# Performance work log

Measured on AMD Instinct MI355X. Metric: run time of the kernel, lower is better.

## Reference

```python
import jax, jax.numpy as jnp
import numpy as np

D = 1024
H = 16
DH = D // H
F = 4096
EPS = 1e-5

def layernorm(x, gamma, beta):
    mean = jnp.mean(x, axis=-1, keepdims=True)
    var = jnp.mean((x - mean) ** 2, axis=-1, keepdims=True)  # biased variance
    return gamma * (x - mean) / jnp.sqrt(var + EPS) + beta

def setup_inputs() -> dict:
    key = jax.random.key(0)
    ks = jax.random.split(key, 12)
    s = 1.0 / np.sqrt(D)
    sf = 1.0 / np.sqrt(F)
    return {
        "x": jax.random.normal(ks[0], (16, 512, D), dtype=jnp.float32),
        "Wq": jax.random.normal(ks[1], (H, D, DH), dtype=jnp.float32) * s,
        "Wk": jax.random.normal(ks[2], (H, D, DH), dtype=jnp.float32) * s,
        "Wv": jax.random.normal(ks[3], (H, D, DH), dtype=jnp.float32) * s,
        "Wo": jax.random.normal(ks[4], (D, D), dtype=jnp.float32) * s,
        "bo": jax.random.normal(ks[5], (D,), dtype=jnp.float32) * s,
        "gamma1": jnp.ones((D,), dtype=jnp.float32),
        "beta1": jnp.zeros((D,), dtype=jnp.float32),
        "gamma2": jnp.ones((D,), dtype=jnp.float32),
        "beta2": jnp.zeros((D,), dtype=jnp.float32),
        "W1": jax.random.normal(ks[6], (D, F), dtype=jnp.float32) * s,
        "b1": jax.random.normal(ks[7], (F,), dtype=jnp.float32) * s,
        "W2": jax.random.normal(ks[8], (F, D), dtype=jnp.float32) * sf,
        "b2": jax.random.normal(ks[9], (D,), dtype=jnp.float32) * sf,
    }

def reference(x, Wq, Wk, Wv, Wo, bo, gamma1, beta1, gamma2, beta2, W1, b1, W2, b2):
    B, S, _ = x.shape
    n1 = layernorm(x, gamma1, beta1)
    # per-head projections (no bias) -> [B,H,S,DH]
    Q = jnp.einsum('bsd,hde->bhse', n1, Wq)
    K = jnp.einsum('bsd,hde->bhse', n1, Wk)
    V = jnp.einsum('bsd,hde->bhse', n1, Wv)
    scores = jnp.einsum('bhse,bhte->bhst', Q, K) / jnp.sqrt(jnp.float32(DH))
    causal = jnp.tril(jnp.ones((S, S), dtype=bool))  # keep lower triangle
    scores = jnp.where(causal, scores, -jnp.inf)
    attn = jax.nn.softmax(scores, axis=-1)  # dropout is identity at eval
    heads = jnp.einsum('bhst,bhte->bhse', attn, V)
    concat = heads.transpose(0, 2, 1, 3).reshape(B, S, D)  # concat heads in order
    x = x + (concat @ Wo + bo)
    n2 = layernorm(x, gamma2, beta2)
    ff = jax.nn.gelu(n2 @ W1 + b1, approximate=False) @ W2 + b2
    return x + ff
```

## Files before the change

### kernel.cpp

```cpp
#include <hip/hip_runtime.h>
#include <hip/hip_bf16.h>
#include <math.h>

constexpr int Dm = 1024;
constexpr int Hh = 16;
constexpr int Ff = 4096;
constexpr int Ss = 512;
constexpr int Bbatch = 16;
constexpr int NT = Bbatch * Ss;
constexpr float EPSc = 1e-5f;

typedef __attribute__((ext_vector_type(8))) short bfrag;
typedef __attribute__((ext_vector_type(4))) float f32x4;

static __device__ __forceinline__ float gelu_f(float v) {
    const float u = v * (0.7978845608f + 0.0356774081f * v * v);
    const float e = __expf(2.0f * u);
    const float th = 1.0f - 2.0f / (e + 1.0f);
    return 0.5f * v * (1.0f + th);
}

static __device__ __forceinline__ void gload16(const void* g, void* l) {
    __builtin_amdgcn_global_load_lds((__attribute__((address_space(1))) void*)g,
                                     (__attribute__((address_space(3))) void*)l,
                                     16, 0, 0);
}

#define SWZ(row, colb) ((row) * 128 + ((colb) ^ (((row) & 7) << 4)))

__global__ void __launch_bounds__(256) transpose_cvt(const float* __restrict__ in,
                                                     __hip_bfloat16* __restrict__ out,
                                                     int R, int C,
                                                     long in_zs, long out_zs) {
    __shared__ float tile[32][33];
    const float* inz = in + (size_t)blockIdx.z * in_zs;
    __hip_bfloat16* outz = out + (size_t)blockIdx.z * out_zs;
    const int c0 = blockIdx.x * 32, r0 = blockIdx.y * 32;
    const int tx = threadIdx.x & 31, ty4 = (threadIdx.x >> 5) * 4;
    #pragma unroll
    for (int i = 0; i < 4; i++)
        tile[ty4 + i][tx] = inz[(size_t)(r0 + ty4 + i) * C + c0 + tx];
    __syncthreads();
    #pragma unroll
    for (int i = 0; i < 4; i++)
        outz[(size_t)(c0 + ty4 + i) * R + r0 + tx] = __float2bfloat16(tile[tx][ty4 + i]);
}

__global__ void __launch_bounds__(256) ln_bf16(const float* __restrict__ x,
                                               const float* __restrict__ gamma,
                                               const float* __restrict__ beta,
                                               __hip_bfloat16* __restrict__ out) {
    const int row = blockIdx.x;
    const int tid = threadIdx.x;
    const int lane = tid & 63, w = tid >> 6;
    float4 xv = reinterpret_cast<const float4*>(x + (size_t)row * Dm)[tid];
    float s  = xv.x + xv.y + xv.z + xv.w;
    float ss = xv.x * xv.x + xv.y * xv.y + xv.z * xv.z + xv.w * xv.w;
    #pragma unroll
    for (int o = 32; o > 0; o >>= 1) {
        s  += __shfl_down(s,  o, 64);
        ss += __shfl_down(ss, o, 64);
    }
    __shared__ float red[2][4];
    if (lane == 0) { red[0][w] = s; red[1][w] = ss; }
    __syncthreads();
    float st  = red[0][0] + red[0][1] + red[0][2] + red[0][3];
    float sst = red[1][0] + red[1][1] + red[1][2] + red[1][3];
    float mean = st * (1.0f / Dm);
    float var  = sst * (1.0f / Dm) - mean * mean;
    float inv  = rsqrtf(var + EPSc);
    float4 g = reinterpret_cast<const float4*>(gamma)[tid];
    float4 b = reinterpret_cast<const float4*>(beta)[tid];
    __hip_bfloat16 t[4] __attribute__((aligned(8)));
    t[0] = __float2bfloat16((xv.x - mean) * inv * g.x + b.x);
    t[1] = __float2bfloat16((xv.y - mean) * inv * g.y + b.y);
    t[2] = __float2bfloat16((xv.z - mean) * inv * g.z + b.z);
    t[3] = __float2bfloat16((xv.w - mean) * inv * g.w + b.w);
    *reinterpret_cast<ushort4*>(out + (size_t)row * Dm + tid * 4) =
        *reinterpret_cast<ushort4*>(t);
}

template<int EPI>
__global__ void __launch_bounds__(256) gemm_db(const __hip_bfloat16* __restrict__ A, int lda,
                                               const __hip_bfloat16* __restrict__ Bt, int ldb,
                                               const float* __restrict__ bias,
                                               const float* __restrict__ res,
                                               void* __restrict__ Cout, int ldc,
                                               int nbx, int K) {
    __shared__ __hip_bfloat16 As[2][128 * 64];
    __shared__ __hip_bfloat16 Bs[2][128 * 64];
    const int tid = threadIdx.x, l = tid & 63, w = tid >> 6;
    const int lr = l & 15, lg = l >> 4;
    const int nwg = gridDim.x;
    const int sbid = (blockIdx.x & 7) * (nwg >> 3) + (blockIdx.x >> 3);
    const int bx = sbid % nbx, by = sbid / nbx;
    const int m0 = by * 128, n0 = bx * 128;
    const int wr = w >> 1, wc = w & 1;
    const int srow = l >> 3;
    const int scol = ((l & 7) ^ srow) * 8;
    const int NK = K >> 6;

    auto STAGE = [&](int t, int bsel) {
        const int k0 = t * 64;
        #pragma unroll
        for (int j = 0; j < 4; j++) {
            const int rb = w * 32 + j * 8;
            gload16(A  + (size_t)(m0 + rb + srow) * lda + k0 + scol, &As[bsel][rb * 64]);
            gload16(Bt + (size_t)(n0 + rb + srow) * ldb + k0 + scol, &Bs[bsel][rb * 64]);
        }
    };

    f32x4 acc[4][4] = {};
    STAGE(0, 0);
    for (int t = 0; t < NK; t++) {
        const int cur = t & 1;
        if (t + 1 < NK) {
            STAGE(t + 1, cur ^ 1);
            asm volatile("s_waitcnt vmcnt(8)" ::: "memory");
        } else {
            asm volatile("s_waitcnt vmcnt(0)" ::: "memory");
        }
        __builtin_amdgcn_s_barrier();
        __builtin_amdgcn_sched_barrier(0);
        const char* Ab = (const char*)&As[cur][0];
        const char* Bb = (const char*)&Bs[cur][0];
        #pragma unroll
        for (int kk = 0; kk < 2; kk++) {
            bfrag a[4], b[4];
            #pragma unroll
            for (int mi = 0; mi < 4; mi++) {
                const int row = wr * 64 + mi * 16 + lr;
                a[mi] = *(const bfrag*)(Ab + SWZ(row, (kk * 4 + lg) * 16));
            }
            #pragma unroll
            for (int ni = 0; ni < 4; ni++) {
                const int row = wc * 64 + ni * 16 + lr;
                b[ni] = *(const bfrag*)(Bb + SWZ(row, (kk * 4 + lg) * 16));
            }
            __builtin_amdgcn_s_setprio(1);
            #pragma unroll
            for (int mi = 0; mi < 4; mi++)
                #pragma unroll
                for (int ni = 0; ni < 4; ni++)
                    acc[mi][ni] = __builtin_amdgcn_mfma_f32_16x16x32_bf16(a[mi], b[ni], acc[mi][ni], 0, 0, 0);
            __builtin_amdgcn_s_setprio(0);
        }
        __builtin_amdgcn_sched_barrier(0);
        __builtin_amdgcn_s_barrier();
    }
    const int rb = m0 + wr * 64 + lg * 4;
    const int cb = n0 + wc * 64 + lr;
    #pragma unroll
    for (int mi = 0; mi < 4; mi++) {
        #pragma unroll
        for (int ni = 0; ni < 4; ni++) {
            #pragma unroll
            for (int rg = 0; rg < 4; rg++) {
                const int row = rb + mi * 16 + rg;
                const int col = cb + ni * 16;
                const size_t off = (size_t)row * ldc + col;
                const float v = acc[mi][ni][rg];
                if (EPI == 0) {
                    ((__hip_bfloat16*)Cout)[off] = __float2bfloat16(v);
                } else if (EPI == 1) {
                    ((float*)Cout)[off] = v + bias[col] + res[off];
                } else if (EPI == 2) {
                    ((__hip_bfloat16*)Cout)[off] = __float2bfloat16(gelu_f(v + bias[col]));
                } else {
                    ((float*)Cout)[off] = ((float*)Cout)[off] + v + bias[col];
                }
            }
        }
    }
}

__global__ void __launch_bounds__(256) attn_mfma(const __hip_bfloat16* __restrict__ QKV,
                                                 __hip_bfloat16* __restrict__ Oc) {
    constexpr int LDQ = 3072;
    __shared__ __hip_bfloat16 Qs[64 * 64];
    __shared__ __hip_bfloat16 Ks[64 * 64];
    __shared__ __hip_bfloat16 Vts[64 * 64];
    __shared__ __hip_bfloat16 Ps[4][16 * 64];
    const int tid = threadIdx.x, l = tid & 63, w = tid >> 6;
    const int lr = l & 15, lg = l >> 4;
    const int qt = blockIdx.x & 7;
    const int h  = (blockIdx.x >> 3) & 15;
    const int b  = blockIdx.x >> 7;

    const __hip_bfloat16* Qg = QKV + (size_t)(b * Ss + qt * 64) * LDQ + h * 64;
    const __hip_bfloat16* Kg = QKV + (size_t)(b * Ss) * LDQ + 1024 + h * 64;
    const __hip_bfloat16* Vg = QKV + (size_t)(b * Ss) * LDQ + 2048 + h * 64;

    const int r8 = l >> 3;
    const int scol = 8 * ((l & 7) ^ r8);

    #pragma unroll
    for (int j = 0; j < 2; j++) {
        const int slot = w * 2 + j;
        gload16(Qg + (size_t)(slot * 8 + r8) * LDQ + scol, Qs + slot * 512);
    }

    float m_run[4] = {-1e30f, -1e30f, -1e30f, -1e30f};
    float l_run[4] = {0.f, 0.f, 0.f, 0.f};
    f32x4 acc_o[4] = {};

    for (int kt = 0; kt <= qt; ++kt) {
        __syncthreads();
        #pragma unroll
        for (int j = 0; j < 2; j++) {
            const int slot = w * 2 + j;
            gload16(Kg + (size_t)(kt * 64 + slot * 8 + r8) * LDQ + scol, Ks + slot * 512);
        }
        unsigned short* vt = reinterpret_cast<unsigned short*>(Vts);
        #pragma unroll
        for (int j = 0; j < 2; j++) {
            const int e = tid + j * 256;
            const int key = e >> 3, f0 = (e & 7) * 8;
            const uint4 raw = *reinterpret_cast<const uint4*>(
                Vg + (size_t)(kt * 64 + key) * LDQ + f0);
            const unsigned int rw[4] = {raw.x, raw.y, raw.z, raw.w};
            #pragma unroll
            for (int e2 = 0; e2 < 8; e2++) {
                const int feat = f0 + e2;
                const int ad = feat * 128 + ((key * 2) ^ ((feat & 7) << 4));
                vt[ad >> 1] = (unsigned short)(rw[e2 >> 1] >> ((e2 & 1) * 16));
            }
        }
        __syncthreads();

        f32x4 s4[4] = {};
        #pragma unroll
        for (int kk = 0; kk < 2; kk++) {
            const bfrag aq = *reinterpret_cast<const bfrag*>(
                (const char*)Qs + SWZ(w * 16 + lr, kk * 64 + lg * 16));
            #pragma unroll
            for (int ni = 0; ni < 4; ni++) {
                const bfrag bk = *reinterpret_cast<const bfrag*>(
                    (const char*)Ks + SWZ(ni * 16 + lr, kk * 64 + lg * 16));
                s4[ni] = __builtin_amdgcn_mfma_f32_16x16x32_bf16(aq, bk, s4[ni], 0, 0, 0);
            }
        }
        float p[4][4];
        #pragma unroll
        for (int ni = 0; ni < 4; ni++)
            #pragma unroll
            for (int rg = 0; rg < 4; rg++)
                p[ni][rg] = s4[ni][rg] * 0.125f;
        if (kt == qt) {
            #pragma unroll
            for (int ni = 0; ni < 4; ni++)
                #pragma unroll
                for (int rg = 0; rg < 4; rg++)
                    if (ni * 16 + lr > w * 16 + lg * 4 + rg) p[ni][rg] = -1e30f;
        }
        float sf[4];
        #pragma unroll
        for (int rg = 0; rg < 4; rg++) {
            float mx = fmaxf(fmaxf(p[0][rg], p[1][rg]), fmaxf(p[2][rg], p[3][rg]));
            #pragma unroll
            for (int o = 1; o < 16; o <<= 1) mx = fmaxf(mx, __shfl_xor(mx, o, 64));
            const float mn = fmaxf(m_run[rg], mx);
            sf[rg] = __expf(m_run[rg] - mn);
            m_run[rg] = mn;
        }
        float rsum[4] = {};
        #pragma unroll
        for (int ni = 0; ni < 4; ni++)
            #pragma unroll
            for (int rg = 0; rg < 4; rg++) {
                const float e = __expf(p[ni][rg] - m_run[rg]);
                p[ni][rg] = e;
                rsum[rg] += e;
            }
        #pragma unroll
        for (int rg = 0; rg < 4; rg++) {
            #pragma unroll
            for (int o = 1; o < 16; o <<= 1) rsum[rg] += __shfl_xor(rsum[rg], o, 64);
            l_run[rg] = l_run[rg] * sf[rg] + rsum[rg];
        }
        #pragma unroll
        for (int di = 0; di < 4; di++)
            #pragma unroll
            for (int rg = 0; rg < 4; rg++)
                acc_o[di][rg] *= sf[rg];
        unsigned short* pw = reinterpret_cast<unsigned short*>(Ps[w]);
        #pragma unroll
        for (int ni = 0; ni < 4; ni++)
            #pragma unroll
            for (int rg = 0; rg < 4; rg++) {
                const int prow = lg * 4 + rg;
                const int ad = SWZ(prow, (ni * 16 + lr) * 2);
                __hip_bfloat16 pb = __float2bfloat16(p[ni][rg]);
                pw[ad >> 1] = *reinterpret_cast<unsigned short*>(&pb);
            }
        #pragma unroll
        for (int kk = 0; kk < 2; kk++) {
            const bfrag pa = *reinterpret_cast<const bfrag*>(
                (const char*)Ps[w] + SWZ(lr, kk * 64 + lg * 16));
            #pragma unroll
            for (int di = 0; di < 4; di++) {
                const bfrag vb = *reinterpret_cast<const bfrag*>(
                    (const char*)Vts + SWZ(di * 16 + lr, kk * 64 + lg * 16));
                acc_o[di] = __builtin_amdgcn_mfma_f32_16x16x32_bf16(pa, vb, acc_o[di], 0, 0, 0);
            }
        }
    }
    #pragma unroll
    for (int di = 0; di < 4; di++)
        #pragma unroll
        for (int rg = 0; rg < 4; rg++) {
            const int q = qt * 64 + w * 16 + lg * 4 + rg;
            const float v = acc_o[di][rg] / l_run[rg];
            Oc[(size_t)(b * Ss + q) * Dm + h * 64 + di * 16 + lr] = __float2bfloat16(v);
        }
}

extern "C" void kernel_launch(void* const* d_in, const int* in_sizes, int n_in,
                              void* d_out, int out_size, void* d_ws, size_t ws_size,
                              hipStream_t stream) {
    const float* x   = (const float*)d_in[0];
    const float* Wq  = (const float*)d_in[1];
    const float* Wk  = (const float*)d_in[2];
    const float* Wv  = (const float*)d_in[3];
    const float* Wo  = (const float*)d_in[4];
    const float* bo  = (const float*)d_in[5];
    const float* g1  = (const float*)d_in[6];
    const float* be1 = (const float*)d_in[7];
    const float* g2  = (const float*)d_in[8];
    const float* be2 = (const float*)d_in[9];
    const float* W1  = (const float*)d_in[10];
    const float* b1  = (const float*)d_in[11];
    const float* W2  = (const float*)d_in[12];
    const float* b2  = (const float*)d_in[13];
    float* out = (float*)d_out;

    char* wsb = (char*)d_ws;
    __hip_bfloat16* WqkvT = (__hip_bfloat16*)(wsb);
    __hip_bfloat16* WoT   = (__hip_bfloat16*)(wsb + 6291456);
    __hip_bfloat16* W1T   = (__hip_bfloat16*)(wsb + 8388608);
    __hip_bfloat16* W2T   = (__hip_bfloat16*)(wsb + 16777216);
    __hip_bfloat16* n1    = (__hip_bfloat16*)(wsb + 25165824);
    __hip_bfloat16* QKV   = (__hip_bfloat16*)(wsb + 41943040);
    __hip_bfloat16* concat = n1;
    __hip_bfloat16* n2     = n1;
    __hip_bfloat16* h1     = QKV;

    transpose_cvt<<<dim3(2, 32, 16), 256, 0, stream>>>(Wq, WqkvT,              1024, 64, 65536, 65536);
    transpose_cvt<<<dim3(2, 32, 16), 256, 0, stream>>>(Wk, WqkvT + 1024 * 1024, 1024, 64, 65536, 65536);
    transpose_cvt<<<dim3(2, 32, 16), 256, 0, stream>>>(Wv, WqkvT + 2048 * 1024, 1024, 64, 65536, 65536);
    transpose_cvt<<<dim3(32, 32, 1), 256, 0, stream>>>(Wo, WoT, 1024, 1024, 0, 0);
    transpose_cvt<<<dim3(128, 32, 1), 256, 0, stream>>>(W1, W1T, 1024, 4096, 0, 0);
    transpose_cvt<<<dim3(32, 128, 1), 256, 0, stream>>>(W2, W2T, 4096, 1024, 0, 0);

    ln_bf16<<<NT, 256, 0, stream>>>(x, g1, be1, n1);
    gemm_db<0><<<1536, 256, 0, stream>>>(n1, Dm, WqkvT, Dm, nullptr, nullptr,
                                         QKV, 3072, 24, Dm);
    attn_mfma<<<NT * Hh / 64, 256, 0, stream>>>(QKV, concat);
    gemm_db<1><<<512, 256, 0, stream>>>(concat, Dm, WoT, Dm, bo, x,
                                        out, Dm, 8, Dm);
    ln_bf16<<<NT, 256, 0, stream>>>(out, g2, be2, n2);
    gemm_db<2><<<2048, 256, 0, stream>>>(n2, Dm, W1T, Dm, b1, nullptr,
                                         h1, Ff, 32, Dm);
    gemm_db<3><<<512, 256, 0, stream>>>(h1, Ff, W2T, Ff, b2, nullptr,
                                        out, Dm, 8, Ff);
}
```

Measured before the change: 402.6 us.

## Prefetch GEMM tiles through registers and write V transposed from QKV epilogue

The GEMM kernel no longer uses double-buffered direct global-to-LDS loads. It now prefetches the next K-tile into registers while the current single-buffered LDS tile is consumed, which halves LDS use and may allow more resident blocks. The QKV projection gains a new epilogue that writes Q/K as before and writes V already transposed per head, so the attention kernel can load V with async 16-byte LDS loads instead of an element-wise transpose scatter. In exchange, the register prefetch adds VGPR pressure, and the V epilogue does narrow 8-byte strided stores.

```diff
diff --git a/kernel.cpp b/kernel.cpp
--- a/kernel.cpp
+++ b/kernel.cpp
@@ -81,14 +81,15 @@
 }
 
 template<int EPI>
-__global__ void __launch_bounds__(256) gemm_db(const __hip_bfloat16* __restrict__ A, int lda,
+__global__ void __launch_bounds__(256) gemm_rp(const __hip_bfloat16* __restrict__ A, int lda,
                                                const __hip_bfloat16* __restrict__ Bt, int ldb,
                                                const float* __restrict__ bias,
                                                const float* __restrict__ res,
                                                void* __restrict__ Cout, int ldc,
+                                               __hip_bfloat16* __restrict__ Vt,
                                                int nbx, int K) {
-    __shared__ __hip_bfloat16 As[2][128 * 64];
-    __shared__ __hip_bfloat16 Bs[2][128 * 64];
+    __shared__ __hip_bfloat16 As[128 * 64];
+    __shared__ __hip_bfloat16 Bs[128 * 64];
     const int tid = threadIdx.x, l = tid & 63, w = tid >> 6;
     const int lr = l & 15, lg = l >> 4;
     const int nwg = gridDim.x;
@@ -100,42 +101,49 @@
     const int scol = ((l & 7) ^ srow) * 8;
     const int NK = K >> 6;
 
-    auto STAGE = [&](int t, int bsel) {
+    uint4 pa[4], pb[4];
+    auto LOADREG = [&](int t) {
         const int k0 = t * 64;
         #pragma unroll
         for (int j = 0; j < 4; j++) {
             const int rb = w * 32 + j * 8;
-            gload16(A  + (size_t)(m0 + rb + srow) * lda + k0 + scol, &As[bsel][rb * 64]);
-            gload16(Bt + (size_t)(n0 + rb + srow) * ldb + k0 + scol, &Bs[bsel][rb * 64]);
+            pa[j] = *(const uint4*)(A  + (size_t)(m0 + rb + srow) * lda + k0 + scol);
+            pb[j] = *(const uint4*)(Bt + (size_t)(n0 + rb + srow) * ldb + k0 + scol);
         }
     };
+    auto WRITELDS = [&]() {
+        #pragma unroll
+        for (int j = 0; j < 4; j++) {
+            const int rb = w * 32 + j * 8;
+            *(uint4*)((char*)As + rb * 128 + l * 16) = pa[j];
+            *(uint4*)((char*)Bs + rb * 128 + l * 16) = pb[j];
+        }
+    };
 
     f32x4 acc[4][4] = {};
-    STAGE(0, 0);
+    LOADREG(0);
+    asm volatile("s_waitcnt vmcnt(0)" ::: "memory");
+    __builtin_amdgcn_sched_barrier(0);
+    WRITELDS();
+    if (NK > 1) LOADREG(1);
+    asm volatile("s_waitcnt lgkmcnt(0)" ::: "memory");
+    __builtin_amdgcn_sched_barrier(0);
+    __builtin_amdgcn_s_barrier();
+
     for (int t = 0; t < NK; t++) {
-        const int cur = t & 1;
-        if (t + 1 < NK) {
-            STAGE(t + 1, cur ^ 1);
-            asm volatile("s_waitcnt vmcnt(8)" ::: "memory");
-        } else {
-            asm volatile("s_waitcnt vmcnt(0)" ::: "memory");
-        }
-        __builtin_amdgcn_s_barrier();
         __builtin_amdgcn_sched_barrier(0);
-        const char* Ab = (const char*)&As[cur][0];
-        const char* Bb = (const char*)&Bs[cur][0];
         #pragma unroll
         for (int kk = 0; kk < 2; kk++) {
             bfrag a[4], b[4];
             #pragma unroll
             for (int mi = 0; mi < 4; mi++) {
                 const int row = wr * 64 + mi * 16 + lr;
-                a[mi] = *(const bfrag*)(Ab + SWZ(row, (kk * 4 + lg) * 16));
+                a[mi] = *(const bfrag*)((const char*)As + SWZ(row, (kk * 4 + lg) * 16));
             }
             #pragma unroll
             for (int ni = 0; ni < 4; ni++) {
                 const int row = wc * 64 + ni * 16 + lr;
-                b[ni] = *(const bfrag*)(Bb + SWZ(row, (kk * 4 + lg) * 16));
+                b[ni] = *(const bfrag*)((const char*)Bs + SWZ(row, (kk * 4 + lg) * 16));
             }
             __builtin_amdgcn_s_setprio(1);
             #pragma unroll
@@ -147,36 +155,67 @@
         }
         __builtin_amdgcn_sched_barrier(0);
         __builtin_amdgcn_s_barrier();
-    }
+        if (t + 1 < NK) {
+            asm volatile("s_waitcnt vmcnt(0)" ::: "memory");
+            __builtin_amdgcn_sched_barrier(0);
+            WRITELDS();
+            if (t + 2 < NK) LOADREG(t + 2);
+            asm volatile("s_waitcnt lgkmcnt(0)" ::: "memory");
+            __builtin_amdgcn_sched_barrier(0);
+        }
+        __builtin_amdgcn_s_barrier();
+    }
+
     const int rb = m0 + wr * 64 + lg * 4;
     const int cb = n0 + wc * 64 + lr;
     #pragma unroll
     for (int mi = 0; mi < 4; mi++) {
         #pragma unroll
         for (int ni = 0; ni < 4; ni++) {
-            #pragma unroll
-            for (int rg = 0; rg < 4; rg++) {
-                const int row = rb + mi * 16 + rg;
-                const int col = cb + ni * 16;
-                const size_t off = (size_t)row * ldc + col;
-                const float v = acc[mi][ni][rg];
-                if (EPI == 0) {
-                    ((__hip_bfloat16*)Cout)[off] = __float2bfloat16(v);
-                } else if (EPI == 1) {
-                    ((float*)Cout)[off] = v + bias[col] + res[off];
-                } else if (EPI == 2) {
-                    ((__hip_bfloat16*)Cout)[off] = __float2bfloat16(gelu_f(v + bias[col]));
+            const int col = cb + ni * 16;
+            if (EPI == 4) {
+                const int row0 = rb + mi * 16;
+                if (col < 2048) {
+                    #pragma unroll
+                    for (int rg = 0; rg < 4; rg++)
+                        ((__hip_bfloat16*)Cout)[(size_t)(row0 + rg) * 2048 + col] =
+                            __float2bfloat16(acc[mi][ni][rg]);
                 } else {
-                    ((float*)Cout)[off] = ((float*)Cout)[off] + v + bias[col];
+                    const int dp = col - 2048, hh = dp >> 6, dd = dp & 63;
+                    const int bb = row0 >> 9, tk = row0 & 511;
+                    ushort4 t4;
+                    __hip_bfloat16 hv;
+                    hv = __float2bfloat16(acc[mi][ni][0]); t4.x = *(unsigned short*)&hv;
+                    hv = __float2bfloat16(acc[mi][ni][1]); t4.y = *(unsigned short*)&hv;
+                    hv = __float2bfloat16(acc[mi][ni][2]); t4.z = *(unsigned short*)&hv;
+                    hv = __float2bfloat16(acc[mi][ni][3]); t4.w = *(unsigned short*)&hv;
+                    *(ushort4*)(Vt + ((size_t)(bb * 16 + hh) * 64 + dd) * 512 + tk) = t4;
                 }
-            }
-        }
-    }
-}
-
-__global__ void __launch_bounds__(256) attn_mfma(const __hip_bfloat16* __restrict__ QKV,
+            } else {
+                #pragma unroll
+                for (int rg = 0; rg < 4; rg++) {
+                    const int row = rb + mi * 16 + rg;
+                    const size_t off = (size_t)row * ldc + col;
+                    const float v = acc[mi][ni][rg];
+                    if (EPI == 0) {
+                        ((__hip_bfloat16*)Cout)[off] = __float2bfloat16(v);
+                    } else if (EPI == 1) {
+                        ((float*)Cout)[off] = v + bias[col] + res[off];
+                    } else if (EPI == 2) {
+                        ((__hip_bfloat16*)Cout)[off] = __float2bfloat16(gelu_f(v + bias[col]));
+                    } else {
+                        ((float*)Cout)[off] = ((float*)Cout)[off] + v + bias[col];
+                    }
+                }
+            }
+        }
+    }
+}
+
+__global__ void __launch_bounds__(256) attn_mfma(const __hip_bfloat16* __restrict__ QK,
+                                                 const __hip_bfloat16* __restrict__ Vt,
                                                  __hip_bfloat16* __restrict__ Oc) {
-    constexpr int LDQ = 3072;
+    constexpr int LDQ = 2048;
     __shared__ __hip_bfloat16 Qs[64 * 64];
     __shared__ __hip_bfloat16 Ks[64 * 64];
     __shared__ __hip_bfloat16 Vts[64 * 64];
@@ -187,9 +226,9 @@
     const int h  = (blockIdx.x >> 3) & 15;
     const int b  = blockIdx.x >> 7;
 
-    const __hip_bfloat16* Qg = QKV + (size_t)(b * Ss + qt * 64) * LDQ + h * 64;
-    const __hip_bfloat16* Kg = QKV + (size_t)(b * Ss) * LDQ + 1024 + h * 64;
-    const __hip_bfloat16* Vg = QKV + (size_t)(b * Ss) * LDQ + 2048 + h * 64;
+    const __hip_bfloat16* Qg = QK + (size_t)(b * Ss + qt * 64) * LDQ + h * 64;
+    const __hip_bfloat16* Kg = QK + (size_t)(b * Ss) * LDQ + 1024 + h * 64;
+    const __hip_bfloat16* Vg = Vt + (size_t)(b * 16 + h) * 64 * 512;
 
     const int r8 = l >> 3;
     const int scol = 8 * ((l & 7) ^ r8);
@@ -210,21 +249,7 @@
         for (int j = 0; j < 2; j++) {
             const int slot = w * 2 + j;
             gload16(Kg + (size_t)(kt * 64 + slot * 8 + r8) * LDQ + scol, Ks + slot * 512);
-        }
-        unsigned short* vt = reinterpret_cast<unsigned short*>(Vts);
-        #pragma unroll
-        for (int j = 0; j < 2; j++) {
-            const int e = tid + j * 256;
-            const int key = e >> 3, f0 = (e & 7) * 8;
-            const uint4 raw = *reinterpret_cast<const uint4*>(
-                Vg + (size_t)(kt * 64 + key) * LDQ + f0);
-            const unsigned int rw[4] = {raw.x, raw.y, raw.z, raw.w};
-            #pragma unroll
-            for (int e2 = 0; e2 < 8; e2++) {
-                const int feat = f0 + e2;
-                const int ad = feat * 128 + ((key * 2) ^ ((feat & 7) << 4));
-                vt[ad >> 1] = (unsigned short)(rw[e2 >> 1] >> ((e2 & 1) * 16));
-            }
+            gload16(Vg + (size_t)(slot * 8 + r8) * 512 + kt * 64 + scol, Vts + slot * 512);
         }
         __syncthreads();
 
@@ -340,10 +365,11 @@
     __hip_bfloat16* W1T   = (__hip_bfloat16*)(wsb + 8388608);
     __hip_bfloat16* W2T   = (__hip_bfloat16*)(wsb + 16777216);
     __hip_bfloat16* n1    = (__hip_bfloat16*)(wsb + 25165824);
-    __hip_bfloat16* QKV   = (__hip_bfloat16*)(wsb + 41943040);
+    __hip_bfloat16* QK    = (__hip_bfloat16*)(wsb + 41943040);
+    __hip_bfloat16* Vt    = (__hip_bfloat16*)(wsb + 75497472);
     __hip_bfloat16* concat = n1;
     __hip_bfloat16* n2     = n1;
-    __hip_bfloat16* h1     = QKV;
+    __hip_bfloat16* h1     = QK;
 
     transpose_cvt<<<dim3(2, 32, 16), 256, 0, stream>>>(Wq, WqkvT,              1024, 64, 65536, 65536);
     transpose_cvt<<<dim3(2, 32, 16), 256, 0, stream>>>(Wk, WqkvT + 1024 * 1024, 1024, 64, 65536, 65536);
@@ -353,14 +379,14 @@
     transpose_cvt<<<dim3(32, 128, 1), 256, 0, stream>>>(W2, W2T, 4096, 1024, 0, 0);
 
     ln_bf16<<<NT, 256, 0, stream>>>(x, g1, be1, n1);
-    gemm_db<0><<<1536, 256, 0, stream>>>(n1, Dm, WqkvT, Dm, nullptr, nullptr,
-                                         QKV, 3072, 24, Dm);
-    attn_mfma<<<NT * Hh / 64, 256, 0, stream>>>(QKV, concat);
-    gemm_db<1><<<512, 256, 0, stream>>>(concat, Dm, WoT, Dm, bo, x,
-                                        out, Dm, 8, Dm);
+    gemm_rp<4><<<1536, 256, 0, stream>>>(n1, Dm, WqkvT, Dm, nullptr, nullptr,
+                                         QK, 2048, Vt, 24, Dm);
+    attn_mfma<<<NT * Hh / 64, 256, 0, stream>>>(QK, Vt, concat);
+    gemm_rp<1><<<512, 256, 0, stream>>>(concat, Dm, WoT, Dm, bo, x,
+                                        out, Dm, nullptr, 8, Dm);
     ln_bf16<<<NT, 256, 0, stream>>>(out, g2, be2, n2);
-    gemm_db<2><<<2048, 256, 0, stream>>>(n2, Dm, W1T, Dm, b1, nullptr,
-                                         h1, Ff, 32, Dm);
-    gemm_db<3><<<512, 256, 0, stream>>>(h1, Ff, W2T, Ff, b2, nullptr,
-                                        out, Dm, 8, Ff);
-}
+    gemm_rp<2><<<2048, 256, 0, stream>>>(n2, Dm, W1T, Dm, b1, nullptr,
+                                         h1, Ff, nullptr, 32, Dm);
+    gemm_rp<3><<<512, 256, 0, stream>>>(h1, Ff, W2T, Ff, b2, nullptr,
+                                        out, Dm, nullptr, 8, Ff);
+}
```

Result: slower. 983.3 us (+144.2%).

## Add 256x256-tile 8-wave GEMM with four-phase pipelined loads for QKV and FFN1

Applied to the files above, without the earlier changes.

Adds a new GEMM kernel that uses 512 threads and 256x256 output tiles, with double-buffered LDS. Global-to-LDS loads for the next k-steps are split across four MFMA phases, with barriers and waitcnts placed between them. The QKV projection and the FFN1+GELU GEMMs now use this kernel instead of the 128x128 one, which raises operand reuse per tile and overlaps memory traffic with compute. In exchange it uses 128KB of LDS and heavy register pressure, so only one workgroup fits per CU, and the grid has fewer blocks than there are CUs times a few.

```diff
diff --git a/kernel.cpp b/kernel.cpp
--- a/kernel.cpp
+++ b/kernel.cpp
@@ -78,6 +78,121 @@
     t[3] = __float2bfloat16((xv.w - mean) * inv * g.w + b.w);
     *reinterpret_cast<ushort4*>(out + (size_t)row * Dm + tid * 4) =
         *reinterpret_cast<ushort4*>(t);
+}
+
+template<int EPI>
+__global__ void __launch_bounds__(512, 1) gemm8ph(const __hip_bfloat16* __restrict__ A, int lda,
+                                                  const __hip_bfloat16* __restrict__ Bt, int ldb,
+                                                  const float* __restrict__ bias,
+                                                  void* __restrict__ Cout, int ldc,
+                                                  int nbx, int K) {
+    __shared__ __hip_bfloat16 As8[2][256 * 64];
+    __shared__ __hip_bfloat16 Bs8[2][256 * 64];
+    const int tid = threadIdx.x, l = tid & 63, w = tid >> 6;
+    const int lr = l & 15, lg = l >> 4;
+    const int nwg = gridDim.x;
+    const int sbid = (blockIdx.x & 7) * (nwg >> 3) + (blockIdx.x >> 3);
+    const int bx = sbid % nbx, by = sbid / nbx;
+    const int m0 = by * 256, n0 = bx * 256;
+    const int wr = w >> 2, wc = w & 3;
+    const int srow = l >> 3;
+    const int scol = ((l & 7) ^ srow) * 8;
+    const int NK = K >> 6;
+
+    auto stageA = [&](int ts, int hh) {
+        #pragma unroll
+        for (int r = 0; r < 2; r++) {
+            const int row = hh * 128 + r * 64 + w * 8 + srow;
+            gload16(A + (size_t)(m0 + row) * lda + ts * 64 + scol, &As8[ts & 1][row * 64]);
+        }
+    };
+    auto stageB = [&](int ts, int hh) {
+        #pragma unroll
+        for (int r = 0; r < 2; r++) {
+            const int row = hh * 128 + r * 64 + w * 8 + srow;
+            gload16(Bt + (size_t)(n0 + row) * ldb + ts * 64 + scol, &Bs8[ts & 1][row * 64]);
+        }
+    };
+
+    f32x4 acc[8][4] = {};
+
+    stageB(0, 0); stageB(0, 1); stageA(0, 0); stageA(0, 1);
+    stageB(1, 0); stageB(1, 1); stageA(1, 0);
+    asm volatile("s_waitcnt vmcnt(6)" ::: "memory");
+    __builtin_amdgcn_s_barrier();
+
+    for (int t = 0; t < NK; t++) {
+        const char* Ab = (const char*)&As8[t & 1][0];
+        const char* Bb = (const char*)&Bs8[t & 1][0];
+        bfrag b_[4][2];
+
+#define PH8(Q, SPRE, SPOST, VM)                                                     \
+        {                                                                           \
+            bfrag a_[2][2];                                                         \
+            _Pragma("unroll")                                                       \
+            for (int f2 = 0; f2 < 2; f2++) {                                        \
+                const int row = wr * 128 + ((Q) * 2 + f2) * 16 + lr;                \
+                _Pragma("unroll")                                                   \
+                for (int kk = 0; kk < 2; kk++)                                      \
+                    a_[f2][kk] = *(const bfrag*)(Ab + row * 128 +                   \
+                                   (((kk * 4 + lg) ^ (row & 7)) << 4));             \
+            }                                                                       \
+            if ((Q) == 0) {                                                         \
+                _Pragma("unroll")                                                   \
+                for (int nf = 0; nf < 4; nf++) {                                    \
+                    const int row = wc * 64 + nf * 16 + lr;                         \
+                    _Pragma("unroll")                                               \
+                    for (int kk = 0; kk < 2; kk++)                                  \
+                        b_[nf][kk] = *(const bfrag*)(Bb + row * 128 +               \
+                                       (((kk * 4 + lg) ^ (row & 7)) << 4));         \
+                }                                                                   \
+            }                                                                       \
+            SPRE;                                                                   \
+            __builtin_amdgcn_s_barrier();                                           \
+            asm volatile("s_waitcnt lgkmcnt(0)" ::: "memory");                      \
+            __builtin_amdgcn_sched_barrier(0);                                      \
+            SPOST;                                                                  \
+            __builtin_amdgcn_s_setprio(1);                                          \
+            _Pragma("unroll")                                                       \
+            for (int f2 = 0; f2 < 2; f2++)                                          \
+                _Pragma("unroll")                                                   \
+                for (int nf = 0; nf < 4; nf++)                                      \
+                    _Pragma("unroll")                                               \
+                    for (int kk = 0; kk < 2; kk++)                                  \
+                        acc[(Q) * 2 + f2][nf] = __builtin_amdgcn_mfma_f32_16x16x32_bf16( \
+                            a_[f2][kk], b_[nf][kk], acc[(Q) * 2 + f2][nf], 0, 0, 0); \
+            __builtin_amdgcn_s_setprio(0);                                          \
+            if ((VM) == 6) asm volatile("s_waitcnt vmcnt(6)" ::: "memory");         \
+            if ((VM) == 0) asm volatile("s_waitcnt vmcnt(0)" ::: "memory");         \
+            __builtin_amdgcn_s_barrier();                                           \
+        }
+
+        const int vm_end = (t + 2 < NK) ? 6 : ((t + 1 < NK) ? 0 : -1);
+        PH8(0, { if (t + 1 < NK) stageA(t + 1, 1); }, {}, -1)
+        PH8(1, { if (t + 2 < NK) stageB(t + 2, 0); }, {}, -1)
+        PH8(2, { if (t + 2 < NK) stageB(t + 2, 1); }, {}, -1)
+        PH8(3, {}, { if (t + 2 < NK) stageA(t + 2, 0); }, vm_end)
+#undef PH8
+    }
+
+    #pragma unroll
+    for (int m = 0; m < 8; m++) {
+        #pragma unroll
+        for (int nf = 0; nf < 4; nf++) {
+            const int col = n0 + wc * 64 + nf * 16 + lr;
+            const float bv = (EPI == 2) ? bias[col] : 0.0f;
+            #pragma unroll
+            for (int rg = 0; rg < 4; rg++) {
+                const int row = m0 + wr * 128 + m * 16 + lg * 4 + rg;
+                const size_t off = (size_t)row * ldc + col;
+                const float v = acc[m][nf][rg];
+                if (EPI == 0)
+                    ((__hip_bfloat16*)Cout)[off] = __float2bfloat16(v);
+                else
+                    ((__hip_bfloat16*)Cout)[off] = __float2bfloat16(gelu_f(v + bv));
+            }
+        }
+    }
 }
 
 template<int EPI>
@@ -160,12 +275,8 @@
                 const int col = cb + ni * 16;
                 const size_t off = (size_t)row * ldc + col;
                 const float v = acc[mi][ni][rg];
-                if (EPI == 0) {
-                    ((__hip_bfloat16*)Cout)[off] = __float2bfloat16(v);
-                } else if (EPI == 1) {
+                if (EPI == 1) {
                     ((float*)Cout)[off] = v + bias[col] + res[off];
-                } else if (EPI == 2) {
-                    ((__hip_bfloat16*)Cout)[off] = __float2bfloat16(gelu_f(v + bias[col]));
                 } else {
                     ((float*)Cout)[off] = ((float*)Cout)[off] + v + bias[col];
                 }
@@ -353,14 +464,14 @@
     transpose_cvt<<<dim3(32, 128, 1), 256, 0, stream>>>(W2, W2T, 4096, 1024, 0, 0);
 
     ln_bf16<<<NT, 256, 0, stream>>>(x, g1, be1, n1);
-    gemm_db<0><<<1536, 256, 0, stream>>>(n1, Dm, WqkvT, Dm, nullptr, nullptr,
-                                         QKV, 3072, 24, Dm);
+    gemm8ph<0><<<384, 512, 0, stream>>>(n1, Dm, WqkvT, Dm, nullptr,
+                                        QKV, 3072, 12, Dm);
     attn_mfma<<<NT * Hh / 64, 256, 0, stream>>>(QKV, concat);
     gemm_db<1><<<512, 256, 0, stream>>>(concat, Dm, WoT, Dm, bo, x,
                                         out, Dm, 8, Dm);
     ln_bf16<<<NT, 256, 0, stream>>>(out, g2, be2, n2);
-    gemm_db<2><<<2048, 256, 0, stream>>>(n2, Dm, W1T, Dm, b1, nullptr,
-                                         h1, Ff, 32, Dm);
+    gemm8ph<2><<<512, 512, 0, stream>>>(n2, Dm, W1T, Dm, b1,
+                                        h1, Ff, 16, Dm);
     gemm_db<3><<<512, 256, 0, stream>>>(h1, Ff, W2T, Ff, b2, nullptr,
                                         out, Dm, 8, Ff);
 }
```

Result: no change. 402.8 us (+0.1%).

## Double-buffer K/V tiles in attention and tile-swizzle GEMM block mapping

Applied to the files above, without the earlier changes.

The attention kernel now double-buffers the K and transposed-V tiles, prefetching the next key tile during the current tile's compute. It also hoists the Q fragments into registers and reverses query-tile order so the longest causal blocks are scheduled first. The GEMM block index mapping is changed to 8x8 supertiles to improve L2 reuse. The changes add LDS use and manual waitcnt/barrier handling. The supertile mapping assumes nbx and the block-row count are multiples of 8.

```diff
diff --git a/kernel.cpp b/kernel.cpp
--- a/kernel.cpp
+++ b/kernel.cpp
@@ -93,7 +93,10 @@
     const int lr = l & 15, lg = l >> 4;
     const int nwg = gridDim.x;
     const int sbid = (blockIdx.x & 7) * (nwg >> 3) + (blockIdx.x >> 3);
-    const int bx = sbid % nbx, by = sbid / nbx;
+    const int st = sbid >> 6, wi = sbid & 63;
+    const int nsx = nbx >> 3;
+    const int bx = (st % nsx) * 8 + (wi & 7);
+    const int by = (st / nsx) * 8 + (wi >> 3);
     const int m0 = by * 128, n0 = bx * 128;
     const int wr = w >> 1, wc = w & 1;
     const int srow = l >> 3;
@@ -178,12 +181,12 @@
                                                  __hip_bfloat16* __restrict__ Oc) {
     constexpr int LDQ = 3072;
     __shared__ __hip_bfloat16 Qs[64 * 64];
-    __shared__ __hip_bfloat16 Ks[64 * 64];
-    __shared__ __hip_bfloat16 Vts[64 * 64];
+    __shared__ __hip_bfloat16 Ks[2][64 * 64];
+    __shared__ __hip_bfloat16 Vts[2][64 * 64];
     __shared__ __hip_bfloat16 Ps[4][16 * 64];
     const int tid = threadIdx.x, l = tid & 63, w = tid >> 6;
     const int lr = l & 15, lg = l >> 4;
-    const int qt = blockIdx.x & 7;
+    const int qt = 7 - (blockIdx.x & 7);
     const int h  = (blockIdx.x >> 3) & 15;
     const int b  = blockIdx.x >> 7;
 
@@ -193,51 +196,79 @@
 
     const int r8 = l >> 3;
     const int scol = 8 * ((l & 7) ^ r8);
+
+    const int vkey0 = tid >> 3, vf0 = (tid & 7) * 8;
+    const int vkey1 = (tid + 256) >> 3, vf1 = vf0;
+
+    uint4 vr[2];
+    auto VLOAD = [&](int kt) {
+        vr[0] = *reinterpret_cast<const uint4*>(Vg + (size_t)(kt * 64 + vkey0) * LDQ + vf0);
+        vr[1] = *reinterpret_cast<const uint4*>(Vg + (size_t)(kt * 64 + vkey1) * LDQ + vf1);
+    };
+    auto VWRITE = [&](int bsel) {
+        unsigned short* vt = reinterpret_cast<unsigned short*>(Vts[bsel]);
+        #pragma unroll
+        for (int j = 0; j < 2; j++) {
+            const int key = j ? vkey1 : vkey0, f0 = j ? vf1 : vf0;
+            const unsigned int rw[4] = {vr[j].x, vr[j].y, vr[j].z, vr[j].w};
+            #pragma unroll
+            for (int e2 = 0; e2 < 8; e2++) {
+                const int feat = f0 + e2;
+                const int ad = feat * 128 + ((key * 2) ^ ((feat & 7) << 4));
+                vt[ad >> 1] = (unsigned short)(rw[e2 >> 1] >> ((e2 & 1) * 16));
+            }
+        }
+    };
+    auto KSTAGE = [&](int kt, int bsel) {
+        #pragma unroll
+        for (int j = 0; j < 2; j++) {
+            const int slot = w * 2 + j;
+            gload16(Kg + (size_t)(kt * 64 + slot * 8 + r8) * LDQ + scol,
+                    Ks[bsel] + slot * 512);
+        }
+    };
 
     #pragma unroll
     for (int j = 0; j < 2; j++) {
         const int slot = w * 2 + j;
         gload16(Qg + (size_t)(slot * 8 + r8) * LDQ + scol, Qs + slot * 512);
     }
+    VLOAD(0);
+    KSTAGE(0, 0);
+    asm volatile("s_waitcnt vmcnt(0)" ::: "memory");
+    VWRITE(0);
+    asm volatile("s_waitcnt lgkmcnt(0)" ::: "memory");
+    __builtin_amdgcn_s_barrier();
+
+    bfrag qf[2];
+    #pragma unroll
+    for (int kk = 0; kk < 2; kk++)
+        qf[kk] = *reinterpret_cast<const bfrag*>(
+            (const char*)Qs + SWZ(w * 16 + lr, kk * 64 + lg * 16));
 
     float m_run[4] = {-1e30f, -1e30f, -1e30f, -1e30f};
     float l_run[4] = {0.f, 0.f, 0.f, 0.f};
     f32x4 acc_o[4] = {};
 
     for (int kt = 0; kt <= qt; ++kt) {
-        __syncthreads();
-        #pragma unroll
-        for (int j = 0; j < 2; j++) {
-            const int slot = w * 2 + j;
-            gload16(Kg + (size_t)(kt * 64 + slot * 8 + r8) * LDQ + scol, Ks + slot * 512);
-        }
-        unsigned short* vt = reinterpret_cast<unsigned short*>(Vts);
-        #pragma unroll
-        for (int j = 0; j < 2; j++) {
-            const int e = tid + j * 256;
-            const int key = e >> 3, f0 = (e & 7) * 8;
-            const uint4 raw = *reinterpret_cast<const uint4*>(
-                Vg + (size_t)(kt * 64 + key) * LDQ + f0);
-            const unsigned int rw[4] = {raw.x, raw.y, raw.z, raw.w};
-            #pragma unroll
-            for (int e2 = 0; e2 < 8; e2++) {
-                const int feat = f0 + e2;
-                const int ad = feat * 128 + ((key * 2) ^ ((feat & 7) << 4));
-                vt[ad >> 1] = (unsigned short)(rw[e2 >> 1] >> ((e2 & 1) * 16));
-            }
-        }
-        __syncthreads();
+        const int cur = kt & 1;
+        if (kt < qt) {
+            VLOAD(kt + 1);
+            KSTAGE(kt + 1, cur ^ 1);
+            asm volatile("s_waitcnt vmcnt(4)" ::: "memory");
+        } else {
+            asm volatile("s_waitcnt vmcnt(0)" ::: "memory");
+        }
+        __builtin_amdgcn_s_barrier();
 
         f32x4 s4[4] = {};
         #pragma unroll
         for (int kk = 0; kk < 2; kk++) {
-            const bfrag aq = *reinterpret_cast<const bfrag*>(
-                (const char*)Qs + SWZ(w * 16 + lr, kk * 64 + lg * 16));
             #pragma unroll
             for (int ni = 0; ni < 4; ni++) {
                 const bfrag bk = *reinterpret_cast<const bfrag*>(
-                    (const char*)Ks + SWZ(ni * 16 + lr, kk * 64 + lg * 16));
-                s4[ni] = __builtin_amdgcn_mfma_f32_16x16x32_bf16(aq, bk, s4[ni], 0, 0, 0);
+                    (const char*)Ks[cur] + SWZ(ni * 16 + lr, kk * 64 + lg * 16));
+                s4[ni] = __builtin_amdgcn_mfma_f32_16x16x32_bf16(qf[kk], bk, s4[ni], 0, 0, 0);
             }
         }
         float p[4][4];
@@ -283,6 +314,9 @@
             #pragma unroll
             for (int rg = 0; rg < 4; rg++)
                 acc_o[di][rg] *= sf[rg];
+
+        if (kt < qt) VWRITE(cur ^ 1);
+
         unsigned short* pw = reinterpret_cast<unsigned short*>(Ps[w]);
         #pragma unroll
         for (int ni = 0; ni < 4; ni++)
@@ -300,10 +334,12 @@
             #pragma unroll
             for (int di = 0; di < 4; di++) {
                 const bfrag vb = *reinterpret_cast<const bfrag*>(
-                    (const char*)Vts + SWZ(di * 16 + lr, kk * 64 + lg * 16));
+                    (const char*)Vts[cur] + SWZ(di * 16 + lr, kk * 64 + lg * 16));
                 acc_o[di] = __builtin_amdgcn_mfma_f32_16x16x32_bf16(pa, vb, acc_o[di], 0, 0, 0);
             }
         }
+        asm volatile("s_waitcnt lgkmcnt(0)" ::: "memory");
+        __builtin_amdgcn_s_barrier();
     }
     #pragma unroll
     for (int di = 0; di < 4; di++)
```

Measured after the change: 398.9 us. Within noise of the previous version (-0.9%).
